# Kernel tuning notes

Hardware: AMD Instinct MI355X
Metric: run time of the kernel (lower is better)

## Reference

```python
import jax, jax.numpy as jnp
import numpy as np

N_NODES = 100000
N_EDGES = 1600000
D_IN = 64
D_OUT = 64


def setup_inputs() -> dict:
    key = jax.random.key(0)
    k1, k2, k3, k4, k5 = jax.random.split(key, 5)
    feat = jax.random.normal(k1, (N_NODES, D_IN), dtype=jnp.float32)
    src = jax.random.randint(k2, (N_EDGES,), 0, N_NODES, dtype=jnp.int64)
    dst = jax.random.randint(k3, (N_EDGES,), 0, N_NODES, dtype=jnp.int64)
    # Xavier-uniform init with relu gain, as in reset_parameters()
    gain = np.sqrt(2.0)
    bound = gain * np.sqrt(6.0 / (D_IN + D_OUT))
    W_self = jax.random.uniform(k4, (D_OUT, D_IN), minval=-bound, maxval=bound, dtype=jnp.float32)
    W_neigh = jax.random.uniform(k5, (D_OUT, D_IN), minval=-bound, maxval=bound, dtype=jnp.float32)
    return {"feat": feat, "src": src, "dst": dst, "W_self": W_self, "W_neigh": W_neigh}


def _spmm_mean(feat, src, dst, n_nodes):
    # Mean neighbor aggregation: for each dst node, average src features.
    gathered = feat[src]  # [E, D] irregular gather
    agg = jax.ops.segment_sum(gathered, dst, num_segments=n_nodes)  # [N, D]
    deg = jax.ops.segment_sum(jnp.ones((src.shape[0],), feat.dtype), dst, num_segments=n_nodes)
    return agg / jnp.maximum(deg, 1.0)[:, None]


def reference(feat, src, dst, W_self, W_neigh):
    neigh = _spmm_mean(feat, src, dst, feat.shape[0])  # [N, D_in]
    # rst = fc_self(feat) + fc_neigh(SpMM(feat))
    return feat @ W_self.T + neigh @ W_neigh.T
```

## Files before the change

kernel.cpp:

```cpp
#include <hip/hip_runtime.h>
#include <hip/hip_fp16.h>

#define N_NODES 100000
#define N_EDGES 1600000
#define D 64
#define ZROW 100000

#define NPB   240
#define NB    417
#define CAP   8192

#define EPB   8192
#define PBLK  ((N_EDGES + EPB - 1) / EPB)
#define CONVB 256

#define W3_FF16     0u
#define W3_PACKED   12800128u
#define W3_GCUR     (W3_PACKED + 4u * NB * CAP)
#define W3_NODEOFF  (W3_GCUR + 4u * NB)
#define W3_NODECNT  (W3_NODEOFF + 4u * N_NODES)
#define W3_W16      (W3_NODECNT + 4u * N_NODES)
#define W3_NEED     (W3_W16 + 16384u)

typedef __attribute__((ext_vector_type(8))) _Float16 half8;
typedef __attribute__((ext_vector_type(4))) float f32x4;

__device__ inline unsigned int h2bits(__half2 h) { return *(unsigned int*)&h; }
__device__ inline __half2 bits2h(unsigned int u) { return *(__half2*)&u; }
__device__ inline __half2 h2shfl_xor(__half2 x, int mask) {
    int i = *(int*)&x;
    i = __shfl_xor(i, mask);
    return *(__half2*)&i;
}

__global__ __launch_bounds__(1024) void k_part_conv(
    const float* __restrict__ feat,
    const int* __restrict__ src, const int* __restrict__ dst,
    const float* __restrict__ Ws, const float* __restrict__ Wn,
    unsigned int* __restrict__ ff16, unsigned int* __restrict__ w16,
    int* __restrict__ gcur, int* __restrict__ packed)
{
    __shared__ int recs[EPB];
    __shared__ int cnt[NB];
    __shared__ int scn[512];
    __shared__ int pos[NB];
    __shared__ int cur[NB];
    __shared__ int dlt[NB];

    const int bid = blockIdx.x;
    const int t   = threadIdx.x;

    if (bid >= PBLK) {
        if (bid < PBLK + CONVB) {
            const int total = N_NODES * D / 8;
            for (int i = (bid - PBLK) * 1024 + t; i < total; i += CONVB * 1024) {
                const float4 x = ((const float4*)feat)[i * 2];
                const float4 y = ((const float4*)feat)[i * 2 + 1];
                uint4 o;
                o.x = h2bits(__floats2half2_rn(x.x, x.y));
                o.y = h2bits(__floats2half2_rn(x.z, x.w));
                o.z = h2bits(__floats2half2_rn(y.x, y.y));
                o.w = h2bits(__floats2half2_rn(y.z, y.w));
                ((uint4*)ff16)[i] = o;
            }
        } else {
            for (int i = t; i < 2048; i += 1024) {
                w16[i]        = h2bits(__floats2half2_rn(Ws[2 * i], Ws[2 * i + 1]));
                w16[2048 + i] = h2bits(__floats2half2_rn(Wn[2 * i], Wn[2 * i + 1]));
            }
            if (t < 32) ff16[ZROW * 32 + t] = 0;
        }
        return;
    }

    const int e0 = bid * EPB;
    const int nE = min(EPB, N_EDGES - e0);

    for (int i = t; i < NB; i += 1024) cnt[i] = 0;
    __syncthreads();

    int pk[8], bk[8];
    #pragma unroll
    for (int k = 0; k < 8; ++k) {
        const int i = t + k * 1024;
        if (i < nE) {
            const int d  = dst[e0 + i];
            const int b  = d / NPB;
            const int dl = d - b * NPB;
            pk[k] = src[e0 + i] | (dl << 17);
            bk[k] = b;
            atomicAdd(&cnt[b], 1);
        } else {
            bk[k] = -1;
        }
    }
    __syncthreads();

    if (t < 512) scn[t] = (t < NB) ? cnt[t] : 0;
    __syncthreads();
    for (int o = 1; o < 512; o <<= 1) {
        int x = 0;
        if (t < 512 && t >= o) x = scn[t - o];
        __syncthreads();
        if (t < 512) scn[t] += x;
        __syncthreads();
    }
    if (t < NB) {
        const int v    = cnt[t];
        const int excl = scn[t] - v;
        pos[t] = excl;
        cur[t] = excl;
        dlt[t] = atomicAdd(&gcur[t], v);
    }
    __syncthreads();

    #pragma unroll
    for (int k = 0; k < 8; ++k) {
        if (bk[k] >= 0) {
            const int p = atomicAdd(&cur[bk[k]], 1);
            recs[p] = pk[k];
        }
    }
    __syncthreads();

    const int w    = t >> 6;
    const int lane = t & 63;
    for (int b = w; b < NB; b += 16) {
        const int n = cnt[b];
        const int o = pos[b];
        const int g = b * CAP + dlt[b];
        for (int i = lane; i < n; i += 64)
            packed[g + i] = recs[o + i];
    }
}

__global__ __launch_bounds__(512) void k_sortb(
    const int* __restrict__ gcur,
    int* packed,
    int* __restrict__ node_off, int* __restrict__ node_cnt)
{
    __shared__ int recs[CAP];
    __shared__ int lcnt[256];
    __shared__ int sc[256];
    __shared__ int lcur[NPB];

    const int t      = threadIdx.x;
    const int bucket = blockIdx.x;
    const int base   = bucket * CAP;
    int total = gcur[bucket];
    if (total > CAP) total = CAP;

    if (t < 256) lcnt[t] = 0;
    __syncthreads();

    for (int i = t; i < total; i += 512) {
        const int r = packed[base + i];
        recs[i] = r;
        atomicAdd(&lcnt[r >> 17], 1);
    }
    __syncthreads();

    if (t < 256) sc[t] = lcnt[t];
    __syncthreads();
    for (int o = 1; o < 256; o <<= 1) {
        int x = 0;
        if (t < 256 && t >= o) x = sc[t - o];
        __syncthreads();
        if (t < 256) sc[t] += x;
        __syncthreads();
    }

    if (t < NPB) {
        const int excl = sc[t] - lcnt[t];
        lcur[t] = excl;
        const int n = bucket * NPB + t;
        if (n < N_NODES) {
            node_off[n] = base + excl;
            node_cnt[n] = lcnt[t];
        }
    }
    __syncthreads();

    for (int i = t; i < total; i += 512) {
        const int r   = recs[i];
        const int pos = atomicAdd(&lcur[r >> 17], 1);
        packed[base + pos] = r & 0x1FFFF;
    }
}

__global__ __launch_bounds__(1024) void k_agg_update(
    const unsigned int* __restrict__ ff16,
    const int* __restrict__ node_off,
    const int* __restrict__ node_cnt,
    const int* __restrict__ packed,
    const _Float16* __restrict__ w16,
    float* __restrict__ out)
{
    __shared__ uint4 meanLDS[16 * 8];

    const int t    = threadIdx.x;
    const int wv   = t >> 6;
    const int lane = t & 63;
    const int n0   = blockIdx.x * 16;
    const int n    = n0 + wv;

    {
        const int start = node_off[n];
        const int deg   = node_cnt[n];
        const int sub   = lane >> 3;
        const int chunk = lane & 7;

        __half2 a0 = __floats2half2_rn(0.f, 0.f);
        __half2 a1 = a0, a2 = a0, a3 = a0;

        for (int b = 0; b < deg; b += 64) {
            const int rem = min(deg - b, 64);
            int p = ZROW;
            if (lane < rem) p = packed[start + b + lane];

            const int npair = (rem + 15) >> 4;
            for (int q = 0; q < npair; ++q) {
                const int e0 = q * 16 + sub;
                const int s0 = __shfl(p, e0)     & 0x1FFFF;
                const int s1 = __shfl(p, e0 + 8) & 0x1FFFF;
                const uint4 v0 = ((const uint4*)ff16)[(size_t)s0 * 8 + chunk];
                const uint4 v1 = ((const uint4*)ff16)[(size_t)s1 * 8 + chunk];
                a0 += bits2h(v0.x);
                a1 += bits2h(v0.y);
                a2 += bits2h(v0.z);
                a3 += bits2h(v0.w);
                a0 += bits2h(v1.x);
                a1 += bits2h(v1.y);
                a2 += bits2h(v1.z);
                a3 += bits2h(v1.w);
            }
        }

        #pragma unroll
        for (int mask = 8; mask <= 32; mask <<= 1) {
            a0 += h2shfl_xor(a0, mask);
            a1 += h2shfl_xor(a1, mask);
            a2 += h2shfl_xor(a2, mask);
            a3 += h2shfl_xor(a3, mask);
        }

        if (lane < 8) {
            const float inv = 1.0f / (float)((deg > 0) ? deg : 1);
            uint4 mb;
            mb.x = h2bits(__floats2half2_rn(__low2float(a0) * inv, __high2float(a0) * inv));
            mb.y = h2bits(__floats2half2_rn(__low2float(a1) * inv, __high2float(a1) * inv));
            mb.z = h2bits(__floats2half2_rn(__low2float(a2) * inv, __high2float(a2) * inv));
            mb.w = h2bits(__floats2half2_rn(__low2float(a3) * inv, __high2float(a3) * inv));
            meanLDS[wv * 8 + (lane ^ (wv & 7))] = mb;
        }
    }
    __syncthreads();

    if (wv != 0) return;

    const int r16 = lane & 15;
    const int g   = lane >> 4;

    half8 bws[4][2], bwn[4][2];
    #pragma unroll
    for (int nt = 0; nt < 4; ++nt) {
        const int c = nt * 16 + r16;
        #pragma unroll
        for (int kt = 0; kt < 2; ++kt) {
            const int k0 = kt * 32 + g * 8;
            bws[nt][kt] = *(const half8*)(w16 + c * 64 + k0);
            bwn[nt][kt] = *(const half8*)(w16 + 4096 + c * 64 + k0);
        }
    }

    f32x4 acc[4] = {{0.f,0.f,0.f,0.f}, {0.f,0.f,0.f,0.f},
                    {0.f,0.f,0.f,0.f}, {0.f,0.f,0.f,0.f}};

    #pragma unroll
    for (int kt = 0; kt < 2; ++kt) {
        const int k8 = kt * 4 + g;
        const uint4 af_u = ((const uint4*)ff16)[(size_t)(n0 + r16) * 8 + k8];
        const uint4 am_u = meanLDS[r16 * 8 + (k8 ^ (r16 & 7))];
        const half8 af = *(const half8*)&af_u;
        const half8 am = *(const half8*)&am_u;
        #pragma unroll
        for (int nt = 0; nt < 4; ++nt) {
            acc[nt] = __builtin_amdgcn_mfma_f32_16x16x32_f16(af, bws[nt][kt], acc[nt], 0, 0, 0);
            acc[nt] = __builtin_amdgcn_mfma_f32_16x16x32_f16(am, bwn[nt][kt], acc[nt], 0, 0, 0);
        }
    }

    #pragma unroll
    for (int nt = 0; nt < 4; ++nt) {
        #pragma unroll
        for (int r = 0; r < 4; ++r) {
            const int ro = n0 + g * 4 + r;
            out[(size_t)ro * 64 + nt * 16 + r16] = acc[nt][r];
        }
    }
}

__global__ __launch_bounds__(256) void sage_scatter(
    const float* __restrict__ feat,
    const int*   __restrict__ src,
    const int*   __restrict__ dst,
    float*       __restrict__ agg,
    float*       __restrict__ deg)
{
    const int gtid = blockIdx.x * blockDim.x + threadIdx.x;
    const int edge = gtid >> 6;
    const int lane = gtid & 63;
    if (edge >= N_EDGES) return;
    const int s = src[edge];
    const int d = dst[edge];
    atomicAdd(&agg[d * D + lane], feat[s * D + lane]);
    if (lane == 0) atomicAdd(&deg[d], 1.0f);
}

#define RL(v, l) __int_as_float(__builtin_amdgcn_readlane(__float_as_int(v), (l)))

__global__ __launch_bounds__(256) void k_update_div(
    const float* __restrict__ feat,
    const float* __restrict__ Ws,
    const float* __restrict__ Wn,
    const float* __restrict__ deg,
    float* out)
{
    const int wid   = (blockIdx.x * 256 + threadIdx.x) >> 6;
    const int lane  = threadIdx.x & 63;
    const int nwave = (gridDim.x * 256) >> 6;

    const float4* Ws4 = (const float4*)Ws;
    const float4* Wn4 = (const float4*)Wn;
    float4 ws[16], wn[16];
    #pragma unroll
    for (int j = 0; j < 16; ++j) {
        ws[j] = Ws4[lane * 16 + j];
        wn[j] = Wn4[lane * 16 + j];
    }

    for (int n = wid; n < N_NODES; n += nwave) {
        const float f = feat[n * D + lane];
        const float a = out[n * D + lane] / fmaxf(deg[n], 1.0f);
        float s0 = 0.f, s1 = 0.f, m0 = 0.f, m1 = 0.f;
        #pragma unroll
        for (int j = 0; j < 16; ++j) {
            const float4 w_s = ws[j];
            const float4 w_n = wn[j];
            s0 = fmaf(RL(f, 4 * j + 0), w_s.x, s0);
            s1 = fmaf(RL(f, 4 * j + 1), w_s.y, s1);
            s0 = fmaf(RL(f, 4 * j + 2), w_s.z, s0);
            s1 = fmaf(RL(f, 4 * j + 3), w_s.w, s1);
            m0 = fmaf(RL(a, 4 * j + 0), w_n.x, m0);
            m1 = fmaf(RL(a, 4 * j + 1), w_n.y, m1);
            m0 = fmaf(RL(a, 4 * j + 2), w_n.z, m0);
            m1 = fmaf(RL(a, 4 * j + 3), w_n.w, m1);
        }
        out[n * D + lane] = (s0 + s1) + (m0 + m1);
    }
}

extern "C" void kernel_launch(void* const* d_in, const int* in_sizes, int n_in,
                              void* d_out, int out_size, void* d_ws, size_t ws_size,
                              hipStream_t stream) {
    const float* feat = (const float*)d_in[0];
    const int*   src  = (const int*)d_in[1];
    const int*   dst  = (const int*)d_in[2];
    const float* Ws   = (const float*)d_in[3];
    const float* Wn   = (const float*)d_in[4];
    float* out = (float*)d_out;
    char*  ws  = (char*)d_ws;

    if (ws_size >= W3_NEED) {
        unsigned int* ff16 = (unsigned int*)(ws + W3_FF16);
        int* packed = (int*)(ws + W3_PACKED);
        int* gcur   = (int*)(ws + W3_GCUR);
        int* noff   = (int*)(ws + W3_NODEOFF);
        int* ncnt   = (int*)(ws + W3_NODECNT);
        unsigned int* w16u = (unsigned int*)(ws + W3_W16);

        hipMemsetAsync(gcur, 0, (size_t)NB * sizeof(int), stream);

        k_part_conv <<<PBLK + CONVB + 1, 1024, 0, stream>>>(
            feat, src, dst, Ws, Wn, ff16, w16u, gcur, packed);
        k_sortb     <<<NB, 512, 0, stream>>>(gcur, packed, noff, ncnt);
        k_agg_update<<<N_NODES / 16, 1024, 0, stream>>>(
            ff16, noff, ncnt, packed, (const _Float16*)w16u, out);
    } else {
        float* deg = (float*)ws;
        hipMemsetAsync(out, 0, (size_t)N_NODES * D * sizeof(float), stream);
        hipMemsetAsync(deg, 0, (size_t)N_NODES * sizeof(float), stream);
        sage_scatter<<<(N_EDGES * 64) / 256, 256, 0, stream>>>(feat, src, dst, out, deg);
        k_update_div<<<1024, 256, 0, stream>>>(feat, Ws, Wn, deg, out);
    }
}
```

Before: 98.02 us.

## Split fused aggregate+MFMA kernel into separate aggregation and update kernels

The fused kernel is replaced by two kernels. The first uses 256-thread blocks with one wave per node to compute each node's fp16 neighbour mean and writes it into the output buffer as scratch. The second reads each row's features and stored mean, runs the MFMA projection with all four waves busy, and overwrites the same rows in place. This removes the block-wide barrier and the phase where 15 of 16 waves sat idle during the matrix multiply. In exchange it adds a kernel launch and an extra round trip of the mean rows through global memory.

After: 98.19 us. About the same (+0.2%).

```diff
diff --git a/kernel.cpp b/kernel.cpp
--- a/kernel.cpp
+++ b/kernel.cpp
@@ -188,78 +188,78 @@
     }
 }
 
-__global__ __launch_bounds__(1024) void k_agg_update(
+__global__ __launch_bounds__(256) void k_agg_f16(
     const unsigned int* __restrict__ ff16,
     const int* __restrict__ node_off,
     const int* __restrict__ node_cnt,
     const int* __restrict__ packed,
+    float* __restrict__ out)
+{
+    const int gtid = blockIdx.x * 256 + threadIdx.x;
+    const int n    = gtid >> 6;
+    const int lane = gtid & 63;
+    if (n >= N_NODES) return;
+
+    const int start = node_off[n];
+    const int deg   = node_cnt[n];
+    const int sub   = lane >> 3;
+    const int chunk = lane & 7;
+
+    __half2 a0 = __floats2half2_rn(0.f, 0.f);
+    __half2 a1 = a0, a2 = a0, a3 = a0;
+
+    for (int b = 0; b < deg; b += 64) {
+        const int rem = min(deg - b, 64);
+        int p = ZROW;
+        if (lane < rem) p = packed[start + b + lane];
+
+        const int npair = (rem + 15) >> 4;
+        for (int q = 0; q < npair; ++q) {
+            const int e0 = q * 16 + sub;
+            const int s0 = __shfl(p, e0)     & 0x1FFFF;
+            const int s1 = __shfl(p, e0 + 8) & 0x1FFFF;
+            const uint4 v0 = ((const uint4*)ff16)[(size_t)s0 * 8 + chunk];
+            const uint4 v1 = ((const uint4*)ff16)[(size_t)s1 * 8 + chunk];
+            a0 += bits2h(v0.x);
+            a1 += bits2h(v0.y);
+            a2 += bits2h(v0.z);
+            a3 += bits2h(v0.w);
+            a0 += bits2h(v1.x);
+            a1 += bits2h(v1.y);
+            a2 += bits2h(v1.z);
+            a3 += bits2h(v1.w);
+        }
+    }
+
+    #pragma unroll
+    for (int mask = 8; mask <= 32; mask <<= 1) {
+        a0 += h2shfl_xor(a0, mask);
+        a1 += h2shfl_xor(a1, mask);
+        a2 += h2shfl_xor(a2, mask);
+        a3 += h2shfl_xor(a3, mask);
+    }
+
+    if (lane < 8) {
+        const float inv = 1.0f / (float)((deg > 0) ? deg : 1);
+        uint4 mb;
+        mb.x = h2bits(__floats2half2_rn(__low2float(a0) * inv, __high2float(a0) * inv));
+        mb.y = h2bits(__floats2half2_rn(__low2float(a1) * inv, __high2float(a1) * inv));
+        mb.z = h2bits(__floats2half2_rn(__low2float(a2) * inv, __high2float(a2) * inv));
+        mb.w = h2bits(__floats2half2_rn(__low2float(a3) * inv, __high2float(a3) * inv));
+        ((uint4*)out)[(size_t)n * 16 + lane] = mb;
+    }
+}
+
+__global__ __launch_bounds__(256) void k_update_mfma(
+    const unsigned int* __restrict__ ff16,
     const _Float16* __restrict__ w16,
-    float* __restrict__ out)
-{
-    __shared__ uint4 meanLDS[16 * 8];
-
-    const int t    = threadIdx.x;
-    const int wv   = t >> 6;
-    const int lane = t & 63;
-    const int n0   = blockIdx.x * 16;
-    const int n    = n0 + wv;
-
-    {
-        const int start = node_off[n];
-        const int deg   = node_cnt[n];
-        const int sub   = lane >> 3;
-        const int chunk = lane & 7;
-
-        __half2 a0 = __floats2half2_rn(0.f, 0.f);
-        __half2 a1 = a0, a2 = a0, a3 = a0;
-
-        for (int b = 0; b < deg; b += 64) {
-            const int rem = min(deg - b, 64);
-            int p = ZROW;
-            if (lane < rem) p = packed[start + b + lane];
-
-            const int npair = (rem + 15) >> 4;
-            for (int q = 0; q < npair; ++q) {
-                const int e0 = q * 16 + sub;
-                const int s0 = __shfl(p, e0)     & 0x1FFFF;
-                const int s1 = __shfl(p, e0 + 8) & 0x1FFFF;
-                const uint4 v0 = ((const uint4*)ff16)[(size_t)s0 * 8 + chunk];
-                const uint4 v1 = ((const uint4*)ff16)[(size_t)s1 * 8 + chunk];
-                a0 += bits2h(v0.x);
-                a1 += bits2h(v0.y);
-                a2 += bits2h(v0.z);
-                a3 += bits2h(v0.w);
-                a0 += bits2h(v1.x);
-                a1 += bits2h(v1.y);
-                a2 += bits2h(v1.z);
-                a3 += bits2h(v1.w);
-            }
-        }
-
-        #pragma unroll
-        for (int mask = 8; mask <= 32; mask <<= 1) {
-            a0 += h2shfl_xor(a0, mask);
-            a1 += h2shfl_xor(a1, mask);
-            a2 += h2shfl_xor(a2, mask);
-            a3 += h2shfl_xor(a3, mask);
-        }
-
-        if (lane < 8) {
-            const float inv = 1.0f / (float)((deg > 0) ? deg : 1);
-            uint4 mb;
-            mb.x = h2bits(__floats2half2_rn(__low2float(a0) * inv, __high2float(a0) * inv));
-            mb.y = h2bits(__floats2half2_rn(__low2float(a1) * inv, __high2float(a1) * inv));
-            mb.z = h2bits(__floats2half2_rn(__low2float(a2) * inv, __high2float(a2) * inv));
-            mb.w = h2bits(__floats2half2_rn(__low2float(a3) * inv, __high2float(a3) * inv));
-            meanLDS[wv * 8 + (lane ^ (wv & 7))] = mb;
-        }
-    }
-    __syncthreads();
-
-    if (wv != 0) return;
-
-    const int r16 = lane & 15;
-    const int g   = lane >> 4;
+    float* out)
+{
+    const int wv   = threadIdx.x >> 6;
+    const int lane = threadIdx.x & 63;
+    const int n0   = blockIdx.x * 64 + wv * 16;
+    const int r16  = lane & 15;
+    const int g    = lane >> 4;
 
     half8 bws[4][2], bwn[4][2];
     #pragma unroll
@@ -273,14 +273,17 @@
         }
     }
 
+    const int arow = n0 + r16;
+    const int rc   = (arow < N_NODES) ? arow : (N_NODES - 1);
+
     f32x4 acc[4] = {{0.f,0.f,0.f,0.f}, {0.f,0.f,0.f,0.f},
                     {0.f,0.f,0.f,0.f}, {0.f,0.f,0.f,0.f}};
 
     #pragma unroll
     for (int kt = 0; kt < 2; ++kt) {
         const int k8 = kt * 4 + g;
-        const uint4 af_u = ((const uint4*)ff16)[(size_t)(n0 + r16) * 8 + k8];
-        const uint4 am_u = meanLDS[r16 * 8 + (k8 ^ (r16 & 7))];
+        const uint4 af_u = ((const uint4*)ff16)[(size_t)rc * 8 + k8];
+        const uint4 am_u = ((const uint4*)out )[(size_t)rc * 16 + k8];
         const half8 af = *(const half8*)&af_u;
         const half8 am = *(const half8*)&am_u;
         #pragma unroll
@@ -295,7 +298,8 @@
         #pragma unroll
         for (int r = 0; r < 4; ++r) {
             const int ro = n0 + g * 4 + r;
-            out[(size_t)ro * 64 + nt * 16 + r16] = acc[nt][r];
+            if (ro < N_NODES)
+                out[(size_t)ro * 64 + nt * 16 + r16] = acc[nt][r];
         }
     }
 }
@@ -381,11 +385,13 @@
 
         hipMemsetAsync(gcur, 0, (size_t)NB * sizeof(int), stream);
 
-        k_part_conv <<<PBLK + CONVB + 1, 1024, 0, stream>>>(
+        k_part_conv  <<<PBLK + CONVB + 1, 1024, 0, stream>>>(
             feat, src, dst, Ws, Wn, ff16, w16u, gcur, packed);
-        k_sortb     <<<NB, 512, 0, stream>>>(gcur, packed, noff, ncnt);
-        k_agg_update<<<N_NODES / 16, 1024, 0, stream>>>(
-            ff16, noff, ncnt, packed, (const _Float16*)w16u, out);
+        k_sortb      <<<NB, 512, 0, stream>>>(gcur, packed, noff, ncnt);
+        k_agg_f16    <<<(N_NODES * 64 + 255) / 256, 256, 0, stream>>>(
+            ff16, noff, ncnt, packed, out);
+        k_update_mfma<<<(N_NODES + 63) / 64, 256, 0, stream>>>(
+            ff16, (const _Float16*)w16u, out);
     } else {
         float* deg = (float*)ws;
         hipMemsetAsync(out, 0, (size_t)N_NODES * D * sizeof(float), stream);
```
